# Optimization experiments

Hardware: AMD Instinct MI355X
Metric: run time of the kernel (lower is better)

The kernel has to match this reference:

```python
import jax, jax.numpy as jnp
import numpy as np

N_NODES = 50000
N_EDGES = 800000
D = 64
H = 128


def setup_inputs() -> dict:
    key = jax.random.key(0)
    ks = jax.random.split(key, 8)
    s = 0.05
    return {
        "nodes": jax.random.normal(ks[0], (N_NODES, D), jnp.float32),
        "edges": jax.random.normal(ks[1], (N_EDGES, D), jnp.float32),
        "We1": jax.random.normal(ks[2], (3 * D, H), jnp.float32) * s,
        "be1": jnp.zeros((H,), jnp.float32),
        "We2": jax.random.normal(ks[3], (H, D), jnp.float32) * s,
        "be2": jnp.zeros((D,), jnp.float32),
        "Wn1": jax.random.normal(ks[4], (2 * D, H), jnp.float32) * s,
        "bn1": jnp.zeros((H,), jnp.float32),
        "Wn2": jax.random.normal(ks[5], (H, D), jnp.float32) * s,
        "bn2": jnp.zeros((D,), jnp.float32),
        "senders": jax.random.randint(ks[6], (N_EDGES,), 0, N_NODES, jnp.int32),
        "receivers": jax.random.randint(ks[7], (N_EDGES,), 0, N_NODES, jnp.int32),
    }


def reference(nodes, edges, We1, be1, We2, be2, Wn1, bn1, Wn2, bn2, senders, receivers):
    # EdgeBlock(use_globals=False): concat[edge, receiver_node, sender_node] -> MLP
    edge_in = jnp.concatenate([edges, nodes[receivers], nodes[senders]], axis=-1)  # [E, 3D]
    h = jax.nn.relu(edge_in @ We1 + be1)
    new_edges = h @ We2 + be2  # [E, D]

    # NodeBlock(use_sent_edges=False, use_globals=False):
    # aggregate received edges via segment_sum, concat with node feats -> MLP
    agg = jax.ops.segment_sum(new_edges, receivers, num_segments=nodes.shape[0])  # [N, D]
    node_in = jnp.concatenate([agg, nodes], axis=-1)  # [N, 2D]
    h2 = jax.nn.relu(node_in @ Wn1 + bn1)
    new_nodes = h2 @ Wn2 + bn2  # [N, D]
    return new_nodes
```

## Files before the change

### kernel.cpp

```cpp
#include <hip/hip_runtime.h>

#define NN 50000
#define NE 800000

typedef __attribute__((ext_vector_type(8))) short bf16x8;
typedef __attribute__((ext_vector_type(8))) unsigned short us8;
typedef __attribute__((ext_vector_type(4))) unsigned short us4;
typedef __attribute__((ext_vector_type(4))) float f32x4;

#define MFMA16 __builtin_amdgcn_mfma_f32_16x16x32_bf16

__device__ __forceinline__ unsigned short f2b(float f) {
    union { float f; unsigned int u; } x; x.f = f;
    unsigned int r = x.u + 0x7FFFu + ((x.u >> 16) & 1u);
    return (unsigned short)(r >> 16);
}

__device__ __forceinline__ void atomic_pk_add_bf16(unsigned short* addr, unsigned int pk) {
    asm volatile("global_atomic_pk_add_bf16 %0, %1, off" :: "v"(addr), "v"(pk) : "memory");
}

__global__ __launch_bounds__(256) void prep_kernel(
    const float* __restrict__ nodes,
    const float* __restrict__ We1, const float* __restrict__ We2,
    const float* __restrict__ Wn1, const float* __restrict__ Wn2,
    unsigned short* __restrict__ nodes_bf,
    unsigned short* __restrict__ We1T, unsigned short* __restrict__ We2T,
    unsigned short* __restrict__ Wn1T, unsigned short* __restrict__ Wn2T)
{
    const int b = blockIdx.x, t = threadIdx.x;
    if (b < 400) {
        const float4* src = (const float4*)nodes;
        for (int i = b * 256 + t; i < NN * 16; i += 400 * 256) {
            float4 v = src[i];
            us4 o; o[0] = f2b(v.x); o[1] = f2b(v.y); o[2] = f2b(v.z); o[3] = f2b(v.w);
            *(us4*)&nodes_bf[(size_t)i * 4] = o;
        }
    } else {
        const int base = (b - 400) * 256 + t;
        for (int idx = base; idx < 57344; idx += 16 * 256) {
            if (idx < 24576) {
                int n = idx / 192, k = idx % 192;
                We1T[idx] = f2b(We1[k * 128 + n]);
            } else if (idx < 32768) {
                int j = idx - 24576; int n = j / 128, k = j % 128;
                We2T[j] = f2b(We2[k * 64 + n]);
            } else if (idx < 49152) {
                int j = idx - 32768; int n = j / 128, k = j % 128;
                Wn1T[j] = f2b(Wn1[k * 128 + n]);
            } else {
                int j = idx - 49152; int n = j / 128, k = j % 128;
                Wn2T[j] = f2b(Wn2[k * 64 + n]);
            }
        }
    }
}

__global__ __launch_bounds__(256, 4) void edge_kernel(
    const unsigned short* __restrict__ nodes_bf, const float* __restrict__ edges,
    const unsigned short* __restrict__ We1T, const float* __restrict__ be1,
    const unsigned short* __restrict__ We2T, const float* __restrict__ be2,
    const int* __restrict__ senders, const int* __restrict__ receivers,
    unsigned short* __restrict__ agg_bf)
{
    __shared__ unsigned short xs[64 * 200];
    __shared__ unsigned short wb[128 * 40];
    __shared__ int ridx[64];
    __shared__ int sidx[64];

    const int t = threadIdx.x;
    const int e0 = blockIdx.x * 64;
    const int w = t >> 6;
    const int l = t & 63;
    const int lc = l & 15;
    const int lq = l >> 4;

    if (t < 64) { ridx[t] = receivers[e0 + t]; sidx[t] = senders[e0 + t]; }
    __syncthreads();

    #pragma unroll
    for (int i = 0; i < 4; ++i) {
        int idx = t + 256 * i;
        int m = idx >> 4, q = idx & 15;
        float4 v = *(const float4*)&edges[((size_t)(e0 + m)) * 64 + q * 4];
        us4 o; o[0] = f2b(v.x); o[1] = f2b(v.y); o[2] = f2b(v.z); o[3] = f2b(v.w);
        *(us4*)&xs[m * 200 + q * 4] = o;
    }
    #pragma unroll
    for (int i = 0; i < 2; ++i) {
        int idx = t + 256 * i;
        int m = idx >> 3, q = idx & 7;
        us8 v = *(const us8*)&nodes_bf[(size_t)ridx[m] * 64 + q * 8];
        *(us8*)&xs[m * 200 + 64 + q * 8] = v;
    }
    #pragma unroll
    for (int i = 0; i < 2; ++i) {
        int idx = t + 256 * i;
        int m = idx >> 3, q = idx & 7;
        us8 v = *(const us8*)&nodes_bf[(size_t)sidx[m] * 64 + q * 8];
        *(us8*)&xs[m * 200 + 128 + q * 8] = v;
    }
    __syncthreads();

    f32x4 acc[4][2];
    #pragma unroll
    for (int mt = 0; mt < 4; ++mt) { acc[mt][0] = (f32x4)0.f; acc[mt][1] = (f32x4)0.f; }

    for (int c = 0; c < 6; ++c) {
        const int k0 = 32 * c;
        #pragma unroll
        for (int i = 0; i < 2; ++i) {
            int idx = t + 256 * i;
            int n = idx >> 2, cc = idx & 3;
            *(us8*)&wb[n * 40 + cc * 8] = *(const us8*)&We1T[n * 192 + k0 + cc * 8];
        }
        __syncthreads();
        bf16x8 b0 = *(const bf16x8*)&wb[(w * 32 + lc) * 40 + lq * 8];
        bf16x8 b1 = *(const bf16x8*)&wb[(w * 32 + 16 + lc) * 40 + lq * 8];
        #pragma unroll
        for (int mt = 0; mt < 4; ++mt) {
            bf16x8 a = *(const bf16x8*)&xs[(mt * 16 + lc) * 200 + k0 + lq * 8];
            acc[mt][0] = MFMA16(a, b0, acc[mt][0], 0, 0, 0);
            acc[mt][1] = MFMA16(a, b1, acc[mt][1], 0, 0, 0);
        }
        __syncthreads();
    }

    #pragma unroll
    for (int nt = 0; nt < 2; ++nt) {
        int col = w * 32 + nt * 16 + lc;
        float bias = be1[col];
        #pragma unroll
        for (int mt = 0; mt < 4; ++mt) {
            #pragma unroll
            for (int r = 0; r < 4; ++r) {
                int row = mt * 16 + lq * 4 + r;
                float v = fmaxf(acc[mt][nt][r] + bias, 0.f);
                xs[row * 136 + col] = f2b(v);
            }
        }
    }
    __syncthreads();

    f32x4 acc2[4];
    #pragma unroll
    for (int mt = 0; mt < 4; ++mt) acc2[mt] = (f32x4)0.f;

    for (int c = 0; c < 4; ++c) {
        const int k0 = 32 * c;
        {
            int n = t >> 2, cc = t & 3;
            *(us8*)&wb[n * 40 + cc * 8] = *(const us8*)&We2T[n * 128 + k0 + cc * 8];
        }
        __syncthreads();
        bf16x8 b = *(const bf16x8*)&wb[(w * 16 + lc) * 40 + lq * 8];
        #pragma unroll
        for (int mt = 0; mt < 4; ++mt) {
            bf16x8 a = *(const bf16x8*)&xs[(mt * 16 + lc) * 136 + k0 + lq * 8];
            acc2[mt] = MFMA16(a, b, acc2[mt], 0, 0, 0);
        }
        __syncthreads();
    }

    float* fs = (float*)xs;
    {
        const int col = w * 16 + lc;
        const float bias2 = be2[col];
        #pragma unroll
        for (int mt = 0; mt < 4; ++mt) {
            #pragma unroll
            for (int r = 0; r < 4; ++r) {
                int row = mt * 16 + lq * 4 + r;
                fs[row * 66 + col] = acc2[mt][r] + bias2;
            }
        }
    }
    __syncthreads();

    #pragma unroll
    for (int i = 0; i < 8; ++i) {
        int p = t + 256 * i;
        int row = p >> 5, cp = p & 31;
        float2 v = *(const float2*)&fs[row * 66 + cp * 2];
        unsigned int pk = (unsigned int)f2b(v.x) | ((unsigned int)f2b(v.y) << 16);
        atomic_pk_add_bf16(&agg_bf[(size_t)ridx[row] * 64 + cp * 2], pk);
    }
}

__global__ __launch_bounds__(256, 4) void node_kernel(
    const unsigned short* __restrict__ nodes_bf, const unsigned short* __restrict__ agg_bf,
    const unsigned short* __restrict__ Wn1T, const float* __restrict__ bn1,
    const unsigned short* __restrict__ Wn2T, const float* __restrict__ bn2,
    float* __restrict__ out)
{
    __shared__ unsigned short xs[64 * 136];
    __shared__ unsigned short wb[128 * 40];

    const int t = threadIdx.x;
    const int n0 = blockIdx.x * 64;
    const int w = t >> 6;
    const int l = t & 63;
    const int lc = l & 15;
    const int lq = l >> 4;

    #pragma unroll
    for (int i = 0; i < 2; ++i) {
        int idx = t + 256 * i;
        int m = idx >> 3, q = idx & 7;
        int n = n0 + m;
        us8 v = {0, 0, 0, 0, 0, 0, 0, 0};
        if (n < NN) v = *(const us8*)&agg_bf[(size_t)n * 64 + q * 8];
        *(us8*)&xs[m * 136 + q * 8] = v;
    }
    #pragma unroll
    for (int i = 0; i < 2; ++i) {
        int idx = t + 256 * i;
        int m = idx >> 3, q = idx & 7;
        int n = n0 + m;
        us8 v = {0, 0, 0, 0, 0, 0, 0, 0};
        if (n < NN) v = *(const us8*)&nodes_bf[(size_t)n * 64 + q * 8];
        *(us8*)&xs[m * 136 + 64 + q * 8] = v;
    }
    __syncthreads();

    f32x4 acc[4][2];
    #pragma unroll
    for (int mt = 0; mt < 4; ++mt) { acc[mt][0] = (f32x4)0.f; acc[mt][1] = (f32x4)0.f; }

    for (int c = 0; c < 4; ++c) {
        const int k0 = 32 * c;
        #pragma unroll
        for (int i = 0; i < 2; ++i) {
            int idx = t + 256 * i;
            int n = idx >> 2, cc = idx & 3;
            *(us8*)&wb[n * 40 + cc * 8] = *(const us8*)&Wn1T[n * 128 + k0 + cc * 8];
        }
        __syncthreads();
        bf16x8 b0 = *(const bf16x8*)&wb[(w * 32 + lc) * 40 + lq * 8];
        bf16x8 b1 = *(const bf16x8*)&wb[(w * 32 + 16 + lc) * 40 + lq * 8];
        #pragma unroll
        for (int mt = 0; mt < 4; ++mt) {
            bf16x8 a = *(const bf16x8*)&xs[(mt * 16 + lc) * 136 + k0 + lq * 8];
            acc[mt][0] = MFMA16(a, b0, acc[mt][0], 0, 0, 0);
            acc[mt][1] = MFMA16(a, b1, acc[mt][1], 0, 0, 0);
        }
        __syncthreads();
    }

    #pragma unroll
    for (int nt = 0; nt < 2; ++nt) {
        int col = w * 32 + nt * 16 + lc;
        float bias = bn1[col];
        #pragma unroll
        for (int mt = 0; mt < 4; ++mt) {
            #pragma unroll
            for (int r = 0; r < 4; ++r) {
                int row = mt * 16 + lq * 4 + r;
                float v = fmaxf(acc[mt][nt][r] + bias, 0.f);
                xs[row * 136 + col] = f2b(v);
            }
        }
    }
    __syncthreads();

    f32x4 acc2[4];
    #pragma unroll
    for (int mt = 0; mt < 4; ++mt) acc2[mt] = (f32x4)0.f;

    for (int c = 0; c < 4; ++c) {
        const int k0 = 32 * c;
        {
            int n = t >> 2, cc = t & 3;
            *(us8*)&wb[n * 40 + cc * 8] = *(const us8*)&Wn2T[n * 128 + k0 + cc * 8];
        }
        __syncthreads();
        bf16x8 b = *(const bf16x8*)&wb[(w * 16 + lc) * 40 + lq * 8];
        #pragma unroll
        for (int mt = 0; mt < 4; ++mt) {
            bf16x8 a = *(const bf16x8*)&xs[(mt * 16 + lc) * 136 + k0 + lq * 8];
            acc2[mt] = MFMA16(a, b, acc2[mt], 0, 0, 0);
        }
        __syncthreads();
    }

    const int col = w * 16 + lc;
    const float bias2 = bn2[col];
    #pragma unroll
    for (int mt = 0; mt < 4; ++mt) {
        #pragma unroll
        for (int r = 0; r < 4; ++r) {
            int row = mt * 16 + lq * 4 + r;
            int n = n0 + row;
            if (n < NN) out[(size_t)n * 64 + col] = acc2[mt][r] + bias2;
        }
    }
}

extern "C" void kernel_launch(void* const* d_in, const int* in_sizes, int n_in,
                              void* d_out, int out_size, void* d_ws, size_t ws_size,
                              hipStream_t stream) {
    const float* nodes = (const float*)d_in[0];
    const float* edges = (const float*)d_in[1];
    const float* We1   = (const float*)d_in[2];
    const float* be1   = (const float*)d_in[3];
    const float* We2   = (const float*)d_in[4];
    const float* be2   = (const float*)d_in[5];
    const float* Wn1   = (const float*)d_in[6];
    const float* bn1   = (const float*)d_in[7];
    const float* Wn2   = (const float*)d_in[8];
    const float* bn2   = (const float*)d_in[9];
    const int* senders   = (const int*)d_in[10];
    const int* receivers = (const int*)d_in[11];
    float* out = (float*)d_out;

    char* ws = (char*)d_ws;
    unsigned short* agg_bf = (unsigned short*)ws;
    unsigned short* nodes_bf = (unsigned short*)(ws + 12800000);
    unsigned short* We1T = (unsigned short*)(ws + 19200000);
    unsigned short* We2T = (unsigned short*)(ws + 19249152);
    unsigned short* Wn1T = (unsigned short*)(ws + 19265536);
    unsigned short* Wn2T = (unsigned short*)(ws + 19298304);

    hipMemsetAsync(agg_bf, 0, (size_t)NN * 64 * sizeof(unsigned short), stream);
    prep_kernel<<<416, 256, 0, stream>>>(nodes, We1, We2, Wn1, Wn2,
                                         nodes_bf, We1T, We2T, Wn1T, Wn2T);
    edge_kernel<<<NE / 64, 256, 0, stream>>>(nodes_bf, edges, We1T, be1, We2T, be2,
                                             senders, receivers, agg_bf);
    node_kernel<<<(NN + 63) / 64, 256, 0, stream>>>(nodes_bf, agg_bf, Wn1T, bn1, Wn2T, bn2, out);
}
```

Before: 421.2 us.

## Replace bf16 atomic scatter with counting-sort placement and segmented node-side reduction

When the workspace is large enough, the receivers are histogrammed and prefix-scanned into CSR offsets. Each edge output row is then written as bf16 to its sorted slot, and the node kernel sums its incoming edge rows in fp32 instead of relying on bf16 packed atomics. Weights are also kept in registers per wave rather than staged through shared memory in chunks, which removes many barriers. The cost is four extra small kernels, a roughly 100MB intermediate buffer of edge outputs (written and read back), and an uneven per-node gather loop in the node kernel.

```diff
diff --git a/kernel.cpp b/kernel.cpp
--- a/kernel.cpp
+++ b/kernel.cpp
@@ -2,6 +2,8 @@
 
 #define NN 50000
 #define NE 800000
+#define NNP 50176
+#define SCANB 196
 
 typedef __attribute__((ext_vector_type(8))) short bf16x8;
 typedef __attribute__((ext_vector_type(8))) unsigned short us8;
@@ -15,7 +17,10 @@
     unsigned int r = x.u + 0x7FFFu + ((x.u >> 16) & 1u);
     return (unsigned short)(r >> 16);
 }
-
+__device__ __forceinline__ float b2f(unsigned short u) {
+    union { unsigned int u; float f; } x; x.u = ((unsigned int)u) << 16;
+    return x.f;
+}
 __device__ __forceinline__ void atomic_pk_add_bf16(unsigned short* addr, unsigned int pk) {
     asm volatile("global_atomic_pk_add_bf16 %0, %1, off" :: "v"(addr), "v"(pk) : "memory");
 }
@@ -56,26 +61,101 @@
     }
 }
 
-__global__ __launch_bounds__(256, 4) void edge_kernel(
+__global__ __launch_bounds__(256) void hist_kernel(
+    const int* __restrict__ receivers, int* __restrict__ deg)
+{
+    int e = blockIdx.x * 256 + threadIdx.x;
+    if (e < NE) atomicAdd(&deg[receivers[e]], 1);
+}
+
+__global__ __launch_bounds__(256) void scan1_kernel(
+    const int* __restrict__ deg, int* __restrict__ psum)
+{
+    __shared__ int red[256];
+    int t = threadIdx.x;
+    red[t] = deg[blockIdx.x * 256 + t];
+    __syncthreads();
+    for (int s = 128; s > 0; s >>= 1) {
+        if (t < s) red[t] += red[t + s];
+        __syncthreads();
+    }
+    if (t == 0) psum[blockIdx.x] = red[0];
+}
+
+__global__ __launch_bounds__(256) void scan2_kernel(
+    const int* __restrict__ psum, int* __restrict__ poff)
+{
+    __shared__ int a[256];
+    int t = threadIdx.x;
+    int v0 = (t < SCANB) ? psum[t] : 0;
+    a[t] = v0;
+    __syncthreads();
+    for (int off = 1; off < 256; off <<= 1) {
+        int x = a[t];
+        if (t >= off) x += a[t - off];
+        __syncthreads();
+        a[t] = x;
+        __syncthreads();
+    }
+    poff[t] = a[t] - v0;
+}
+
+__global__ __launch_bounds__(256) void scan3_kernel(
+    const int* __restrict__ deg, const int* __restrict__ poff, int* __restrict__ basep)
+{
+    __shared__ int a[256];
+    int t = threadIdx.x, i = blockIdx.x * 256 + t;
+    int v0 = deg[i];
+    a[t] = v0;
+    __syncthreads();
+    for (int off = 1; off < 256; off <<= 1) {
+        int x = a[t];
+        if (t >= off) x += a[t - off];
+        __syncthreads();
+        a[t] = x;
+        __syncthreads();
+    }
+    basep[i] = poff[blockIdx.x] + a[t] - v0;
+}
+
+template<int MODE>
+__global__ __launch_bounds__(256, 4) void edge_kernel_t(
     const unsigned short* __restrict__ nodes_bf, const float* __restrict__ edges,
     const unsigned short* __restrict__ We1T, const float* __restrict__ be1,
     const unsigned short* __restrict__ We2T, const float* __restrict__ be2,
     const int* __restrict__ senders, const int* __restrict__ receivers,
-    unsigned short* __restrict__ agg_bf)
-{
-    __shared__ unsigned short xs[64 * 200];
-    __shared__ unsigned short wb[128 * 40];
+    const int* __restrict__ basep, int* __restrict__ cursor,
+    unsigned short* __restrict__ sorted_e, unsigned short* __restrict__ agg_bf)
+{
+    __shared__ __align__(16) unsigned short xs[64 * 200];
     __shared__ int ridx[64];
     __shared__ int sidx[64];
+    __shared__ int wpos[64];
 
     const int t = threadIdx.x;
     const int e0 = blockIdx.x * 64;
-    const int w = t >> 6;
-    const int l = t & 63;
-    const int lc = l & 15;
-    const int lq = l >> 4;
-
-    if (t < 64) { ridx[t] = receivers[e0 + t]; sidx[t] = senders[e0 + t]; }
+    const int w = t >> 6, l = t & 63, lc = l & 15, lq = l >> 4;
+
+    int myr = -1;
+    if (t < 64) {
+        myr = receivers[e0 + t];
+        ridx[t] = myr;
+        sidx[t] = senders[e0 + t];
+    }
+
+    bf16x8 wA0[6], wA1[6], wB[4];
+    #pragma unroll
+    for (int c = 0; c < 6; ++c) {
+        wA0[c] = *(const bf16x8*)&We1T[(w * 32 + lc) * 192 + c * 32 + lq * 8];
+        wA1[c] = *(const bf16x8*)&We1T[(w * 32 + 16 + lc) * 192 + c * 32 + lq * 8];
+    }
+    #pragma unroll
+    for (int c = 0; c < 4; ++c)
+        wB[c] = *(const bf16x8*)&We2T[(w * 16 + lc) * 128 + c * 32 + lq * 8];
+    const float b1x = be1[w * 32 + lc];
+    const float b1y = be1[w * 32 + 16 + lc];
+    const float bias2 = be2[w * 16 + lc];
+
     __syncthreads();
 
     #pragma unroll
@@ -100,36 +180,27 @@
         us8 v = *(const us8*)&nodes_bf[(size_t)sidx[m] * 64 + q * 8];
         *(us8*)&xs[m * 200 + 128 + q * 8] = v;
     }
+    if (MODE == 0 && t < 64) wpos[t] = basep[myr] + atomicAdd(&cursor[myr], 1);
     __syncthreads();
 
     f32x4 acc[4][2];
     #pragma unroll
     for (int mt = 0; mt < 4; ++mt) { acc[mt][0] = (f32x4)0.f; acc[mt][1] = (f32x4)0.f; }
-
+    #pragma unroll
     for (int c = 0; c < 6; ++c) {
-        const int k0 = 32 * c;
-        #pragma unroll
-        for (int i = 0; i < 2; ++i) {
-            int idx = t + 256 * i;
-            int n = idx >> 2, cc = idx & 3;
-            *(us8*)&wb[n * 40 + cc * 8] = *(const us8*)&We1T[n * 192 + k0 + cc * 8];
-        }
-        __syncthreads();
-        bf16x8 b0 = *(const bf16x8*)&wb[(w * 32 + lc) * 40 + lq * 8];
-        bf16x8 b1 = *(const bf16x8*)&wb[(w * 32 + 16 + lc) * 40 + lq * 8];
-        #pragma unroll
-        for (int mt = 0; mt < 4; ++mt) {
-            bf16x8 a = *(const bf16x8*)&xs[(mt * 16 + lc) * 200 + k0 + lq * 8];
-            acc[mt][0] = MFMA16(a, b0, acc[mt][0], 0, 0, 0);
-            acc[mt][1] = MFMA16(a, b1, acc[mt][1], 0, 0, 0);
-        }
-        __syncthreads();
-    }
+        #pragma unroll
+        for (int mt = 0; mt < 4; ++mt) {
+            bf16x8 a = *(const bf16x8*)&xs[(mt * 16 + lc) * 200 + c * 32 + lq * 8];
+            acc[mt][0] = MFMA16(a, wA0[c], acc[mt][0], 0, 0, 0);
+            acc[mt][1] = MFMA16(a, wA1[c], acc[mt][1], 0, 0, 0);
+        }
+    }
+    __syncthreads();
 
     #pragma unroll
     for (int nt = 0; nt < 2; ++nt) {
         int col = w * 32 + nt * 16 + lc;
-        float bias = be1[col];
+        float bias = nt ? b1y : b1x;
         #pragma unroll
         for (int mt = 0; mt < 4; ++mt) {
             #pragma unroll
@@ -145,72 +216,121 @@
     f32x4 acc2[4];
     #pragma unroll
     for (int mt = 0; mt < 4; ++mt) acc2[mt] = (f32x4)0.f;
-
+    #pragma unroll
     for (int c = 0; c < 4; ++c) {
-        const int k0 = 32 * c;
-        {
-            int n = t >> 2, cc = t & 3;
-            *(us8*)&wb[n * 40 + cc * 8] = *(const us8*)&We2T[n * 128 + k0 + cc * 8];
-        }
-        __syncthreads();
-        bf16x8 b = *(const bf16x8*)&wb[(w * 16 + lc) * 40 + lq * 8];
-        #pragma unroll
-        for (int mt = 0; mt < 4; ++mt) {
-            bf16x8 a = *(const bf16x8*)&xs[(mt * 16 + lc) * 136 + k0 + lq * 8];
-            acc2[mt] = MFMA16(a, b, acc2[mt], 0, 0, 0);
-        }
-        __syncthreads();
-    }
+        #pragma unroll
+        for (int mt = 0; mt < 4; ++mt) {
+            bf16x8 a = *(const bf16x8*)&xs[(mt * 16 + lc) * 136 + c * 32 + lq * 8];
+            acc2[mt] = MFMA16(a, wB[c], acc2[mt], 0, 0, 0);
+        }
+    }
+    __syncthreads();
 
     float* fs = (float*)xs;
     {
         const int col = w * 16 + lc;
-        const float bias2 = be2[col];
         #pragma unroll
         for (int mt = 0; mt < 4; ++mt) {
             #pragma unroll
             for (int r = 0; r < 4; ++r) {
                 int row = mt * 16 + lq * 4 + r;
-                fs[row * 66 + col] = acc2[mt][r] + bias2;
+                fs[row * 68 + col] = acc2[mt][r] + bias2;
             }
         }
     }
     __syncthreads();
 
-    #pragma unroll
-    for (int i = 0; i < 8; ++i) {
-        int p = t + 256 * i;
-        int row = p >> 5, cp = p & 31;
-        float2 v = *(const float2*)&fs[row * 66 + cp * 2];
-        unsigned int pk = (unsigned int)f2b(v.x) | ((unsigned int)f2b(v.y) << 16);
-        atomic_pk_add_bf16(&agg_bf[(size_t)ridx[row] * 64 + cp * 2], pk);
-    }
-}
-
-__global__ __launch_bounds__(256, 4) void node_kernel(
-    const unsigned short* __restrict__ nodes_bf, const unsigned short* __restrict__ agg_bf,
+    if (MODE == 0) {
+        int g = t >> 3, l8 = t & 7;
+        #pragma unroll
+        for (int k = 0; k < 2; ++k) {
+            int row = g * 2 + k;
+            size_t p = (size_t)wpos[row];
+            float4 va = *(const float4*)&fs[row * 68 + l8 * 8];
+            float4 vb = *(const float4*)&fs[row * 68 + l8 * 8 + 4];
+            us8 o;
+            o[0] = f2b(va.x); o[1] = f2b(va.y); o[2] = f2b(va.z); o[3] = f2b(va.w);
+            o[4] = f2b(vb.x); o[5] = f2b(vb.y); o[6] = f2b(vb.z); o[7] = f2b(vb.w);
+            *(us8*)&sorted_e[p * 64 + l8 * 8] = o;
+        }
+    } else {
+        #pragma unroll
+        for (int i = 0; i < 8; ++i) {
+            int p = t + 256 * i;
+            int row = p >> 5, cp = p & 31;
+            float2 v = *(const float2*)&fs[row * 68 + cp * 2];
+            unsigned int pk = (unsigned int)f2b(v.x) | ((unsigned int)f2b(v.y) << 16);
+            atomic_pk_add_bf16(&agg_bf[(size_t)ridx[row] * 64 + cp * 2], pk);
+        }
+    }
+}
+
+template<int MODE>
+__global__ __launch_bounds__(256, 4) void node_kernel_t(
+    const unsigned short* __restrict__ nodes_bf,
+    const unsigned short* __restrict__ src,
+    const int* __restrict__ basep,
     const unsigned short* __restrict__ Wn1T, const float* __restrict__ bn1,
     const unsigned short* __restrict__ Wn2T, const float* __restrict__ bn2,
     float* __restrict__ out)
 {
-    __shared__ unsigned short xs[64 * 136];
-    __shared__ unsigned short wb[128 * 40];
+    __shared__ __align__(16) unsigned short xs[64 * 136];
+    __shared__ __align__(16) float aggs[(MODE == 0) ? 64 * 64 : 4];
+    __shared__ int nbase[65];
 
     const int t = threadIdx.x;
     const int n0 = blockIdx.x * 64;
-    const int w = t >> 6;
-    const int l = t & 63;
-    const int lc = l & 15;
-    const int lq = l >> 4;
-
-    #pragma unroll
-    for (int i = 0; i < 2; ++i) {
-        int idx = t + 256 * i;
-        int m = idx >> 3, q = idx & 7;
-        int n = n0 + m;
-        us8 v = {0, 0, 0, 0, 0, 0, 0, 0};
-        if (n < NN) v = *(const us8*)&agg_bf[(size_t)n * 64 + q * 8];
-        *(us8*)&xs[m * 136 + q * 8] = v;
+    const int w = t >> 6, l = t & 63, lc = l & 15, lq = l >> 4;
+
+    bf16x8 wA0[4], wA1[4], wB[4];
+    #pragma unroll
+    for (int c = 0; c < 4; ++c) {
+        wA0[c] = *(const bf16x8*)&Wn1T[(w * 32 + lc) * 128 + c * 32 + lq * 8];
+        wA1[c] = *(const bf16x8*)&Wn1T[(w * 32 + 16 + lc) * 128 + c * 32 + lq * 8];
+        wB[c]  = *(const bf16x8*)&Wn2T[(w * 16 + lc) * 128 + c * 32 + lq * 8];
+    }
+    const float b1x = bn1[w * 32 + lc];
+    const float b1y = bn1[w * 32 + 16 + lc];
+    const float bias2 = bn2[w * 16 + lc];
+
+    if (MODE == 0) {
+        if (t < 65) nbase[t] = basep[n0 + t];
+        __syncthreads();
+        int g = t >> 3, l8 = t & 7;
+        #pragma unroll
+        for (int k = 0; k < 2; ++k) {
+            int ln = 2 * g + k, n = n0 + ln;
+            float s0 = 0.f, s1 = 0.f, s2 = 0.f, s3 = 0.f, s4 = 0.f, s5 = 0.f, s6 = 0.f, s7 = 0.f;
+            if (n < NN) {
+                int js = nbase[ln], je = nbase[ln + 1];
+                for (int j = js; j < je; ++j) {
+                    us8 v = *(const us8*)&src[(size_t)j * 64 + l8 * 8];
+                    s0 += b2f(v[0]); s1 += b2f(v[1]); s2 += b2f(v[2]); s3 += b2f(v[3]);
+                    s4 += b2f(v[4]); s5 += b2f(v[5]); s6 += b2f(v[6]); s7 += b2f(v[7]);
+                }
+            }
+            *(float4*)&aggs[ln * 64 + l8 * 8]     = make_float4(s0, s1, s2, s3);
+            *(float4*)&aggs[ln * 64 + l8 * 8 + 4] = make_float4(s4, s5, s6, s7);
+        }
+        __syncthreads();
+        #pragma unroll
+        for (int i = 0; i < 4; ++i) {
+            int idx = t + 256 * i;
+            int m = idx >> 4, q = idx & 15;
+            float4 v = *(const float4*)&aggs[m * 64 + q * 4];
+            us4 o; o[0] = f2b(v.x); o[1] = f2b(v.y); o[2] = f2b(v.z); o[3] = f2b(v.w);
+            *(us4*)&xs[m * 136 + q * 4] = o;
+        }
+    } else {
+        #pragma unroll
+        for (int i = 0; i < 2; ++i) {
+            int idx = t + 256 * i;
+            int m = idx >> 3, q = idx & 7;
+            int n = n0 + m;
+            us8 v = {0, 0, 0, 0, 0, 0, 0, 0};
+            if (n < NN) v = *(const us8*)&src[(size_t)n * 64 + q * 8];
+            *(us8*)&xs[m * 136 + q * 8] = v;
+        }
     }
     #pragma unroll
     for (int i = 0; i < 2; ++i) {
@@ -226,31 +346,21 @@
     f32x4 acc[4][2];
     #pragma unroll
     for (int mt = 0; mt < 4; ++mt) { acc[mt][0] = (f32x4)0.f; acc[mt][1] = (f32x4)0.f; }
-
+    #pragma unroll
     for (int c = 0; c < 4; ++c) {
-        const int k0 = 32 * c;
-        #pragma unroll
-        for (int i = 0; i < 2; ++i) {
-            int idx = t + 256 * i;
-            int n = idx >> 2, cc = idx & 3;
-            *(us8*)&wb[n * 40 + cc * 8] = *(const us8*)&Wn1T[n * 128 + k0 + cc * 8];
-        }
-        __syncthreads();
-        bf16x8 b0 = *(const bf16x8*)&wb[(w * 32 + lc) * 40 + lq * 8];
-        bf16x8 b1 = *(const bf16x8*)&wb[(w * 32 + 16 + lc) * 40 + lq * 8];
-        #pragma unroll
-        for (int mt = 0; mt < 4; ++mt) {
-            bf16x8 a = *(const bf16x8*)&xs[(mt * 16 + lc) * 136 + k0 + lq * 8];
-            acc[mt][0] = MFMA16(a, b0, acc[mt][0], 0, 0, 0);
-            acc[mt][1] = MFMA16(a, b1, acc[mt][1], 0, 0, 0);
-        }
-        __syncthreads();
-    }
+        #pragma unroll
+        for (int mt = 0; mt < 4; ++mt) {
+            bf16x8 a = *(const bf16x8*)&xs[(mt * 16 + lc) * 136 + c * 32 + lq * 8];
+            acc[mt][0] = MFMA16(a, wA0[c], acc[mt][0], 0, 0, 0);
+            acc[mt][1] = MFMA16(a, wA1[c], acc[mt][1], 0, 0, 0);
+        }
+    }
+    __syncthreads();
 
     #pragma unroll
     for (int nt = 0; nt < 2; ++nt) {
         int col = w * 32 + nt * 16 + lc;
-        float bias = bn1[col];
+        float bias = nt ? b1y : b1x;
         #pragma unroll
         for (int mt = 0; mt < 4; ++mt) {
             #pragma unroll
@@ -266,25 +376,16 @@
     f32x4 acc2[4];
     #pragma unroll
     for (int mt = 0; mt < 4; ++mt) acc2[mt] = (f32x4)0.f;
-
+    #pragma unroll
     for (int c = 0; c < 4; ++c) {
-        const int k0 = 32 * c;
-        {
-            int n = t >> 2, cc = t & 3;
-            *(us8*)&wb[n * 40 + cc * 8] = *(const us8*)&Wn2T[n * 128 + k0 + cc * 8];
-        }
-        __syncthreads();
-        bf16x8 b = *(const bf16x8*)&wb[(w * 16 + lc) * 40 + lq * 8];
-        #pragma unroll
-        for (int mt = 0; mt < 4; ++mt) {
-            bf16x8 a = *(const bf16x8*)&xs[(mt * 16 + lc) * 136 + k0 + lq * 8];
-            acc2[mt] = MFMA16(a, b, acc2[mt], 0, 0, 0);
-        }
-        __syncthreads();
+        #pragma unroll
+        for (int mt = 0; mt < 4; ++mt) {
+            bf16x8 a = *(const bf16x8*)&xs[(mt * 16 + lc) * 136 + c * 32 + lq * 8];
+            acc2[mt] = MFMA16(a, wB[c], acc2[mt], 0, 0, 0);
+        }
     }
 
     const int col = w * 16 + lc;
-    const float bias2 = bn2[col];
     #pragma unroll
     for (int mt = 0; mt < 4; ++mt) {
         #pragma unroll
@@ -312,19 +413,51 @@
     const int* senders   = (const int*)d_in[10];
     const int* receivers = (const int*)d_in[11];
     float* out = (float*)d_out;
-
     char* ws = (char*)d_ws;
-    unsigned short* agg_bf = (unsigned short*)ws;
-    unsigned short* nodes_bf = (unsigned short*)(ws + 12800000);
-    unsigned short* We1T = (unsigned short*)(ws + 19200000);
-    unsigned short* We2T = (unsigned short*)(ws + 19249152);
-    unsigned short* Wn1T = (unsigned short*)(ws + 19265536);
-    unsigned short* Wn2T = (unsigned short*)(ws + 19298304);
-
-    hipMemsetAsync(agg_bf, 0, (size_t)NN * 64 * sizeof(unsigned short), stream);
-    prep_kernel<<<416, 256, 0, stream>>>(nodes, We1, We2, Wn1, Wn2,
-                                         nodes_bf, We1T, We2T, Wn1T, Wn2T);
-    edge_kernel<<<NE / 64, 256, 0, stream>>>(nodes_bf, edges, We1T, be1, We2T, be2,
-                                             senders, receivers, agg_bf);
-    node_kernel<<<(NN + 63) / 64, 256, 0, stream>>>(nodes_bf, agg_bf, Wn1T, bn1, Wn2T, bn2, out);
-}
+
+    const size_t NEED = 109518144;
+
+    if (ws_size >= NEED) {
+        unsigned short* sorted_e = (unsigned short*)ws;
+        unsigned short* nodes_bf = (unsigned short*)(ws + 102400000);
+        unsigned short* We1T = (unsigned short*)(ws + 108800000);
+        unsigned short* We2T = (unsigned short*)(ws + 108849152);
+        unsigned short* Wn1T = (unsigned short*)(ws + 108865536);
+        unsigned short* Wn2T = (unsigned short*)(ws + 108898304);
+        int* deg    = (int*)(ws + 108914688);
+        int* basep  = (int*)(ws + 109115392);
+        int* cursor = (int*)(ws + 109316096);
+        int* psum   = (int*)(ws + 109516096);
+        int* poff   = (int*)(ws + 109517120);
+
+        hipMemsetAsync(deg, 0, NNP * sizeof(int), stream);
+        hipMemsetAsync(cursor, 0, NN * sizeof(int), stream);
+        prep_kernel<<<416, 256, 0, stream>>>(nodes, We1, We2, Wn1, Wn2,
+                                             nodes_bf, We1T, We2T, Wn1T, Wn2T);
+        hist_kernel<<<(NE + 255) / 256, 256, 0, stream>>>(receivers, deg);
+        scan1_kernel<<<SCANB, 256, 0, stream>>>(deg, psum);
+        scan2_kernel<<<1, 256, 0, stream>>>(psum, poff);
+        scan3_kernel<<<SCANB, 256, 0, stream>>>(deg, poff, basep);
+        edge_kernel_t<0><<<NE / 64, 256, 0, stream>>>(
+            nodes_bf, edges, We1T, be1, We2T, be2, senders, receivers,
+            basep, cursor, sorted_e, (unsigned short*)nullptr);
+        node_kernel_t<0><<<(NN + 63) / 64, 256, 0, stream>>>(
+            nodes_bf, sorted_e, basep, Wn1T, bn1, Wn2T, bn2, out);
+    } else {
+        unsigned short* agg_bf = (unsigned short*)ws;
+        unsigned short* nodes_bf = (unsigned short*)(ws + 12800000);
+        unsigned short* We1T = (unsigned short*)(ws + 19200000);
+        unsigned short* We2T = (unsigned short*)(ws + 19249152);
+        unsigned short* Wn1T = (unsigned short*)(ws + 19265536);
+        unsigned short* Wn2T = (unsigned short*)(ws + 19298304);
+
+        hipMemsetAsync(agg_bf, 0, (size_t)NN * 64 * sizeof(unsigned short), stream);
+        prep_kernel<<<416, 256, 0, stream>>>(nodes, We1, We2, Wn1, Wn2,
+                                             nodes_bf, We1T, We2T, Wn1T, Wn2T);
+        edge_kernel_t<1><<<NE / 64, 256, 0, stream>>>(
+            nodes_bf, edges, We1T, be1, We2T, be2, senders, receivers,
+            (const int*)nullptr, (int*)nullptr, (unsigned short*)nullptr, agg_bf);
+        node_kernel_t<1><<<(NN + 63) / 64, 256, 0, stream>>>(
+            nodes_bf, agg_bf, (const int*)nullptr, Wn1T, bn1, Wn2T, bn2, out);
+    }
+}
```

Measured after the change: 476.8 us. 1.13x slower.

## Keep MLP weight fragments in registers instead of staging through LDS

Applied to the files above, without the earlier changes.

Each wave now loads its slice of the bf16 weight matrices straight from global memory into registers once at kernel start. This removes the per-chunk LDS weight staging buffer and the two barriers per K-chunk in both GEMMs of the edge and node kernels. Dropping the LDS buffer frees shared memory, so the launch bounds rise to 6 blocks per SIMD, and the fp32 staging stride changes from 66 to 68. The trade-off is higher register pressure from holding 16 weight vectors per lane, which could cause spills under the tighter occupancy bound.

```diff
diff --git a/kernel.cpp b/kernel.cpp
--- a/kernel.cpp
+++ b/kernel.cpp
@@ -56,26 +56,39 @@
     }
 }
 
-__global__ __launch_bounds__(256, 4) void edge_kernel(
+__global__ __launch_bounds__(256, 6) void edge_kernel(
     const unsigned short* __restrict__ nodes_bf, const float* __restrict__ edges,
     const unsigned short* __restrict__ We1T, const float* __restrict__ be1,
     const unsigned short* __restrict__ We2T, const float* __restrict__ be2,
     const int* __restrict__ senders, const int* __restrict__ receivers,
     unsigned short* __restrict__ agg_bf)
 {
-    __shared__ unsigned short xs[64 * 200];
-    __shared__ unsigned short wb[128 * 40];
+    __shared__ __align__(16) unsigned short xs[64 * 200];
     __shared__ int ridx[64];
     __shared__ int sidx[64];
 
     const int t = threadIdx.x;
     const int e0 = blockIdx.x * 64;
-    const int w = t >> 6;
-    const int l = t & 63;
-    const int lc = l & 15;
-    const int lq = l >> 4;
-
-    if (t < 64) { ridx[t] = receivers[e0 + t]; sidx[t] = senders[e0 + t]; }
+    const int w = t >> 6, l = t & 63, lc = l & 15, lq = l >> 4;
+
+    if (t < 64) {
+        ridx[t] = receivers[e0 + t];
+        sidx[t] = senders[e0 + t];
+    }
+
+    bf16x8 wA0[6], wA1[6], wB[4];
+    #pragma unroll
+    for (int c = 0; c < 6; ++c) {
+        wA0[c] = *(const bf16x8*)&We1T[(w * 32 + lc) * 192 + c * 32 + lq * 8];
+        wA1[c] = *(const bf16x8*)&We1T[(w * 32 + 16 + lc) * 192 + c * 32 + lq * 8];
+    }
+    #pragma unroll
+    for (int c = 0; c < 4; ++c)
+        wB[c] = *(const bf16x8*)&We2T[(w * 16 + lc) * 128 + c * 32 + lq * 8];
+    const float b1x = be1[w * 32 + lc];
+    const float b1y = be1[w * 32 + 16 + lc];
+    const float bias2 = be2[w * 16 + lc];
+
     __syncthreads();
 
     #pragma unroll
@@ -105,31 +118,21 @@
     f32x4 acc[4][2];
     #pragma unroll
     for (int mt = 0; mt < 4; ++mt) { acc[mt][0] = (f32x4)0.f; acc[mt][1] = (f32x4)0.f; }
-
+    #pragma unroll
     for (int c = 0; c < 6; ++c) {
-        const int k0 = 32 * c;
-        #pragma unroll
-        for (int i = 0; i < 2; ++i) {
-            int idx = t + 256 * i;
-            int n = idx >> 2, cc = idx & 3;
-            *(us8*)&wb[n * 40 + cc * 8] = *(const us8*)&We1T[n * 192 + k0 + cc * 8];
-        }
-        __syncthreads();
-        bf16x8 b0 = *(const bf16x8*)&wb[(w * 32 + lc) * 40 + lq * 8];
-        bf16x8 b1 = *(const bf16x8*)&wb[(w * 32 + 16 + lc) * 40 + lq * 8];
-        #pragma unroll
-        for (int mt = 0; mt < 4; ++mt) {
-            bf16x8 a = *(const bf16x8*)&xs[(mt * 16 + lc) * 200 + k0 + lq * 8];
-            acc[mt][0] = MFMA16(a, b0, acc[mt][0], 0, 0, 0);
-            acc[mt][1] = MFMA16(a, b1, acc[mt][1], 0, 0, 0);
-        }
-        __syncthreads();
-    }
+        #pragma unroll
+        for (int mt = 0; mt < 4; ++mt) {
+            bf16x8 a = *(const bf16x8*)&xs[(mt * 16 + lc) * 200 + c * 32 + lq * 8];
+            acc[mt][0] = MFMA16(a, wA0[c], acc[mt][0], 0, 0, 0);
+            acc[mt][1] = MFMA16(a, wA1[c], acc[mt][1], 0, 0, 0);
+        }
+    }
+    __syncthreads();
 
     #pragma unroll
     for (int nt = 0; nt < 2; ++nt) {
         int col = w * 32 + nt * 16 + lc;
-        float bias = be1[col];
+        float bias = nt ? b1y : b1x;
         #pragma unroll
         for (int mt = 0; mt < 4; ++mt) {
             #pragma unroll
@@ -145,33 +148,25 @@
     f32x4 acc2[4];
     #pragma unroll
     for (int mt = 0; mt < 4; ++mt) acc2[mt] = (f32x4)0.f;
-
+    #pragma unroll
     for (int c = 0; c < 4; ++c) {
-        const int k0 = 32 * c;
-        {
-            int n = t >> 2, cc = t & 3;
-            *(us8*)&wb[n * 40 + cc * 8] = *(const us8*)&We2T[n * 128 + k0 + cc * 8];
-        }
-        __syncthreads();
-        bf16x8 b = *(const bf16x8*)&wb[(w * 16 + lc) * 40 + lq * 8];
-        #pragma unroll
-        for (int mt = 0; mt < 4; ++mt) {
-            bf16x8 a = *(const bf16x8*)&xs[(mt * 16 + lc) * 136 + k0 + lq * 8];
-            acc2[mt] = MFMA16(a, b, acc2[mt], 0, 0, 0);
-        }
-        __syncthreads();
-    }
+        #pragma unroll
+        for (int mt = 0; mt < 4; ++mt) {
+            bf16x8 a = *(const bf16x8*)&xs[(mt * 16 + lc) * 136 + c * 32 + lq * 8];
+            acc2[mt] = MFMA16(a, wB[c], acc2[mt], 0, 0, 0);
+        }
+    }
+    __syncthreads();
 
     float* fs = (float*)xs;
     {
         const int col = w * 16 + lc;
-        const float bias2 = be2[col];
         #pragma unroll
         for (int mt = 0; mt < 4; ++mt) {
             #pragma unroll
             for (int r = 0; r < 4; ++r) {
                 int row = mt * 16 + lq * 4 + r;
-                fs[row * 66 + col] = acc2[mt][r] + bias2;
+                fs[row * 68 + col] = acc2[mt][r] + bias2;
             }
         }
     }
@@ -181,27 +176,34 @@
     for (int i = 0; i < 8; ++i) {
         int p = t + 256 * i;
         int row = p >> 5, cp = p & 31;
-        float2 v = *(const float2*)&fs[row * 66 + cp * 2];
+        float2 v = *(const float2*)&fs[row * 68 + cp * 2];
         unsigned int pk = (unsigned int)f2b(v.x) | ((unsigned int)f2b(v.y) << 16);
         atomic_pk_add_bf16(&agg_bf[(size_t)ridx[row] * 64 + cp * 2], pk);
     }
 }
 
-__global__ __launch_bounds__(256, 4) void node_kernel(
+__global__ __launch_bounds__(256, 6) void node_kernel(
     const unsigned short* __restrict__ nodes_bf, const unsigned short* __restrict__ agg_bf,
     const unsigned short* __restrict__ Wn1T, const float* __restrict__ bn1,
     const unsigned short* __restrict__ Wn2T, const float* __restrict__ bn2,
     float* __restrict__ out)
 {
-    __shared__ unsigned short xs[64 * 136];
-    __shared__ unsigned short wb[128 * 40];
+    __shared__ __align__(16) unsigned short xs[64 * 136];
 
     const int t = threadIdx.x;
     const int n0 = blockIdx.x * 64;
-    const int w = t >> 6;
-    const int l = t & 63;
-    const int lc = l & 15;
-    const int lq = l >> 4;
+    const int w = t >> 6, l = t & 63, lc = l & 15, lq = l >> 4;
+
+    bf16x8 wA0[4], wA1[4], wB[4];
+    #pragma unroll
+    for (int c = 0; c < 4; ++c) {
+        wA0[c] = *(const bf16x8*)&Wn1T[(w * 32 + lc) * 128 + c * 32 + lq * 8];
+        wA1[c] = *(const bf16x8*)&Wn1T[(w * 32 + 16 + lc) * 128 + c * 32 + lq * 8];
+        wB[c]  = *(const bf16x8*)&Wn2T[(w * 16 + lc) * 128 + c * 32 + lq * 8];
+    }
+    const float b1x = bn1[w * 32 + lc];
+    const float b1y = bn1[w * 32 + 16 + lc];
+    const float bias2 = bn2[w * 16 + lc];
 
     #pragma unroll
     for (int i = 0; i < 2; ++i) {
@@ -226,31 +228,21 @@
     f32x4 acc[4][2];
     #pragma unroll
     for (int mt = 0; mt < 4; ++mt) { acc[mt][0] = (f32x4)0.f; acc[mt][1] = (f32x4)0.f; }
-
+    #pragma unroll
     for (int c = 0; c < 4; ++c) {
-        const int k0 = 32 * c;
-        #pragma unroll
-        for (int i = 0; i < 2; ++i) {
-            int idx = t + 256 * i;
-            int n = idx >> 2, cc = idx & 3;
-            *(us8*)&wb[n * 40 + cc * 8] = *(const us8*)&Wn1T[n * 128 + k0 + cc * 8];
-        }
-        __syncthreads();
-        bf16x8 b0 = *(const bf16x8*)&wb[(w * 32 + lc) * 40 + lq * 8];
-        bf16x8 b1 = *(const bf16x8*)&wb[(w * 32 + 16 + lc) * 40 + lq * 8];
-        #pragma unroll
-        for (int mt = 0; mt < 4; ++mt) {
-            bf16x8 a = *(const bf16x8*)&xs[(mt * 16 + lc) * 136 + k0 + lq * 8];
-            acc[mt][0] = MFMA16(a, b0, acc[mt][0], 0, 0, 0);
-            acc[mt][1] = MFMA16(a, b1, acc[mt][1], 0, 0, 0);
-        }
-        __syncthreads();
-    }
+        #pragma unroll
+        for (int mt = 0; mt < 4; ++mt) {
+            bf16x8 a = *(const bf16x8*)&xs[(mt * 16 + lc) * 136 + c * 32 + lq * 8];
+            acc[mt][0] = MFMA16(a, wA0[c], acc[mt][0], 0, 0, 0);
+            acc[mt][1] = MFMA16(a, wA1[c], acc[mt][1], 0, 0, 0);
+        }
+    }
+    __syncthreads();
 
     #pragma unroll
     for (int nt = 0; nt < 2; ++nt) {
         int col = w * 32 + nt * 16 + lc;
-        float bias = bn1[col];
+        float bias = nt ? b1y : b1x;
         #pragma unroll
         for (int mt = 0; mt < 4; ++mt) {
             #pragma unroll
@@ -266,25 +258,16 @@
     f32x4 acc2[4];
     #pragma unroll
     for (int mt = 0; mt < 4; ++mt) acc2[mt] = (f32x4)0.f;
-
+    #pragma unroll
     for (int c = 0; c < 4; ++c) {
-        const int k0 = 32 * c;
-        {
-            int n = t >> 2, cc = t & 3;
-            *(us8*)&wb[n * 40 + cc * 8] = *(const us8*)&Wn2T[n * 128 + k0 + cc * 8];
-        }
-        __syncthreads();
-        bf16x8 b = *(const bf16x8*)&wb[(w * 16 + lc) * 40 + lq * 8];
-        #pragma unroll
-        for (int mt = 0; mt < 4; ++mt) {
-            bf16x8 a = *(const bf16x8*)&xs[(mt * 16 + lc) * 136 + k0 + lq * 8];
-            acc2[mt] = MFMA16(a, b, acc2[mt], 0, 0, 0);
-        }
-        __syncthreads();
+        #pragma unroll
+        for (int mt = 0; mt < 4; ++mt) {
+            bf16x8 a = *(const bf16x8*)&xs[(mt * 16 + lc) * 136 + c * 32 + lq * 8];
+            acc2[mt] = MFMA16(a, wB[c], acc2[mt], 0, 0, 0);
+        }
     }
 
     const int col = w * 16 + lc;
-    const float bias2 = bn2[col];
     #pragma unroll
     for (int mt = 0; mt < 4; ++mt) {
         #pragma unroll
```

Result: slower. 508.4 us (+20.7%).
